# Performance work log

Hardware: AMD Instinct MI355X
Metric: run time of the kernel (lower is better)

## Reference

```python
import jax, jax.numpy as jnp
import numpy as np
from functools import partial

B, T, F = 4096, 256, 32
H1, H2, NT = 64, 32, 3


def _lstm_layer(x, W_ih, W_hh, b_ih, b_hh):
    """Torch-style LSTM (batch_first). x: [B,T,Fin], W_ih: [4H,Fin], W_hh: [4H,H].
    Gate order i, f, g, o. Returns all hidden states [B,T,H]."""
    Bsz = x.shape[0]
    H = W_hh.shape[1]
    # Precompute input contribution for all timesteps (one big GEMM)
    xg = jnp.einsum('btf,gf->btg', x, W_ih) + b_ih + b_hh  # [B,T,4H]

    def step(carry, xg_t):
        h, c = carry
        gates = xg_t + h @ W_hh.T  # [B,4H]
        i, f, g, o = jnp.split(gates, 4, axis=-1)
        i = jax.nn.sigmoid(i)
        f = jax.nn.sigmoid(f)
        g = jnp.tanh(g)
        o = jax.nn.sigmoid(o)
        c = f * c + i * g
        h = o * jnp.tanh(c)
        return (h, c), h

    init = (jnp.zeros((Bsz, H), x.dtype), jnp.zeros((Bsz, H), x.dtype))
    _, hs = jax.lax.scan(step, init, jnp.swapaxes(xg, 0, 1))  # hs: [T,B,H]
    return jnp.swapaxes(hs, 0, 1)


def setup_inputs() -> dict:
    key = jax.random.key(0)
    ks = jax.random.split(key, 12)
    s1 = 1.0 / np.sqrt(H1)
    s2 = 1.0 / np.sqrt(H2)
    u = lambda k, shape, s: jax.random.uniform(k, shape, jnp.float32, -s, s)
    return {
        'x': jax.random.normal(ks[0], (B, T, F), jnp.float32),
        'W_ih1': u(ks[1], (4 * H1, F), s1),
        'W_hh1': u(ks[2], (4 * H1, H1), s1),
        'b_ih1': u(ks[3], (4 * H1,), s1),
        'b_hh1': u(ks[4], (4 * H1,), s1),
        'W_ih2': u(ks[5], (4 * H2, H1), s2),
        'W_hh2': u(ks[6], (4 * H2, H2), s2),
        'b_ih2': u(ks[7], (4 * H2,), s2),
        'b_hh2': u(ks[8], (4 * H2,), s2),
        'W_head': u(ks[9], (NT, H2), s2),
        'b_head': u(ks[10], (NT,), s2),
    }


def reference(x, W_ih1, W_hh1, b_ih1, b_hh1, W_ih2, W_hh2, b_ih2, b_hh2, W_head, b_head):
    h1 = _lstm_layer(x, W_ih1, W_hh1, b_ih1, b_hh1)   # [B,T,64]; dropout is identity in eval
    h2 = _lstm_layer(h1, W_ih2, W_hh2, b_ih2, b_hh2)  # [B,T,32]
    last = h2[:, -1, :]                               # [B,32]
    return last @ W_head.T + b_head                   # [B,3]
```

## Files before the change

### kernel.cpp

```cpp
#include <hip/hip_runtime.h>

#define Bsz 4096
#define Tt  256
#define Ff  32
#define H1  64
#define H2  32
#define NTAPS 3
#define BT  16
#define NTHR 512
#define CH  16

typedef _Float16 half8  __attribute__((ext_vector_type(8)));
typedef __fp16   fp16x2 __attribute__((ext_vector_type(2)));
typedef float    f32x4  __attribute__((ext_vector_type(4)));

#define H1S 72
#define H2S 40
#define HDS 33

__device__ __forceinline__ float lstm_unit(float pi, float pf, float pg, float po,
                                           float& c) {
    const float K1 = 1.4426950408889634f;
    float ei = __builtin_amdgcn_exp2f(-K1 * pi);
    float ef = __builtin_amdgcn_exp2f(-K1 * pf);
    float eg = __builtin_amdgcn_exp2f(-2.0f * K1 * __builtin_fabsf(pg));
    float eo = __builtin_amdgcn_exp2f(-K1 * po);
    float p1 = (1.0f + ei) * (1.0f + eg);
    float pf1 = 1.0f + ef;
    float R  = __builtin_amdgcn_rcpf(p1 * pf1);
    float t1 = c * p1;
    float t2 = __builtin_copysignf(1.0f - eg, pg) * pf1;
    c = (t1 + t2) * R;
    float ec = __builtin_amdgcn_exp2f(-2.0f * K1 * __builtin_fabsf(c));
    float th = (1.0f - ec) * __builtin_amdgcn_rcpf((1.0f + eo) * (1.0f + ec));
    return __builtin_copysignf(th, c);
}

#define MFMA16(a, b, c) __builtin_amdgcn_mfma_f32_16x16x32_f16((a), (b), (c), 0, 0, 0)

__device__ __forceinline__ void dma16(const float* gp, const float* lp) {
    __builtin_amdgcn_global_load_lds(
        (const __attribute__((address_space(1))) void*)gp,
        (__attribute__((address_space(3))) void*)lp, 16, 0, 0);
}

__device__ __forceinline__ half8 cvt8(f32x4 lo, f32x4 hi) {
    union { half8 v; fp16x2 h[4]; } ax;
    ax.h[0] = __builtin_amdgcn_cvt_pkrtz(lo[0], lo[1]);
    ax.h[1] = __builtin_amdgcn_cvt_pkrtz(lo[2], lo[3]);
    ax.h[2] = __builtin_amdgcn_cvt_pkrtz(hi[0], hi[1]);
    ax.h[3] = __builtin_amdgcn_cvt_pkrtz(hi[2], hi[3]);
    return ax.v;
}

__global__ __launch_bounds__(NTHR, 2)
void lstm2_fused(const float* __restrict__ x,
                 const float* __restrict__ Wih1, const float* __restrict__ Whh1,
                 const float* __restrict__ bih1, const float* __restrict__ bhh1,
                 const float* __restrict__ Wih2, const float* __restrict__ Whh2,
                 const float* __restrict__ bih2, const float* __restrict__ bhh2,
                 const float* __restrict__ Whead, const float* __restrict__ bhead,
                 float* __restrict__ out)
{
    __shared__ __align__(16) _Float16 sH1[2][BT][H1S];
    __shared__ __align__(16) _Float16 sH2[2][BT][H2S];
    __shared__ __align__(16) float    sXC[2][CH][8][BT][4];
    __shared__ __align__(16) float    sXG[2][4][4][64][4];
    __shared__ __align__(16) float    sHead[BT][HDS];

    const int tid  = threadIdx.x;
    const int wid  = tid >> 6;
    const int lane = tid & 63;
    const int l15  = lane & 15;
    const int q    = lane >> 4;
    const int b0   = blockIdx.x * BT;
    const int u    = wid & 3;
    const bool isL1 = (wid < 4);

    const int hT = u & 1, rh = u >> 1;
    const int colL1 = u * 16 + l15;

    const int bL  = lane & 15;
    const int f4b = lane >> 4;
    const float* gbase = x + (size_t)(b0 + bL) * Tt * Ff;

    if (!isL1) {
        #pragma unroll
        for (int j = 0; j < 4; ++j) {
            int tl = u * 4 + j;
            #pragma unroll
            for (int h = 0; h < 2; ++h)
                dma16(gbase + (size_t)tl * Ff + (h * 4 + f4b) * 4,
                      &sXC[0][tl][h * 4][0][0]);
        }
    }

    half8 wA[4][3];
    half8 wX[4];
    float biasA[4], biasX[4];
    if (isL1) {
        #pragma unroll
        for (int G = 0; G < 4; ++G) {
            int gr = G * 64 + colL1;
            #pragma unroll
            for (int c = 0; c < 2; ++c) {
                half8 v;
                #pragma unroll
                for (int e = 0; e < 8; ++e)
                    v[e] = (_Float16)Whh1[gr * H1 + c * 32 + q * 8 + e];
                wA[G][c] = v;
            }
            wA[G][2] = wA[G][1];
            biasA[G] = 0.0f;
            biasX[G] = 0.0f;
        }
    } else {
        #pragma unroll
        for (int G = 0; G < 4; ++G) {
            int gr2 = G * 32 + hT * 16 + l15;
            half8 v0, v1, v2, vx;
            #pragma unroll
            for (int e = 0; e < 8; ++e) {
                int k = q * 8 + e;
                v0[e] = (_Float16)Whh2[gr2 * H2 + k];
                v1[e] = (_Float16)Wih2[gr2 * H1 + k];
                v2[e] = (_Float16)Wih2[gr2 * H1 + 32 + k];
            }
            wA[G][0] = v0; wA[G][1] = v1; wA[G][2] = v2;
            biasA[G] = bih2[gr2] + bhh2[gr2];

            int grx = G * 64 + u * 16 + l15;
            #pragma unroll
            for (int e = 0; e < 8; ++e)
                vx[e] = (_Float16)Wih1[grx * Ff + q * 8 + e];
            wX[G] = vx;
            biasX[G] = bih1[grx] + bhh1[grx];
        }
    }

    for (int idx = tid; idx < BT * H1S; idx += NTHR) ((_Float16*)sH1[1])[idx] = (_Float16)0.0f;
    for (int idx = tid; idx < BT * H2S; idx += NTHR) ((_Float16*)sH2[1])[idx] = (_Float16)0.0f;

    __syncthreads();

    if (!isL1) {
        f32x4 lo = *(const f32x4*)&sXC[0][0][2 * q][l15][0];
        f32x4 hi = *(const f32x4*)&sXC[0][0][2 * q + 1][l15][0];
        half8 ax = cvt8(lo, hi);
        #pragma unroll
        for (int G = 0; G < 4; ++G) {
            f32x4 a = {biasX[G], biasX[G], biasX[G], biasX[G]};
            a = MFMA16(ax, wX[G], a);
            *(f32x4*)&sXG[0][u][G][lane][0] = a;
        }
    }
    __syncthreads();

    float cs0 = 0.0f, cs1 = 0.0f, cs2 = 0.0f, cs3 = 0.0f;

    #pragma unroll 2
    for (int i = 0; i < Tt; ++i) {
        const int cur = i & 1, nxt = cur ^ 1;
        const int cbuf = (i >> 4) & 1;

        if (!isL1 && (i & (CH - 1)) == 0 && i + CH < Tt) {
            const float* gb = gbase + (size_t)(i + CH) * Ff;
            #pragma unroll
            for (int j = 0; j < 4; ++j) {
                int tl = u * 4 + j;
                #pragma unroll
                for (int h = 0; h < 2; ++h)
                    dma16(gb + (size_t)tl * Ff + (h * 4 + f4b) * 4,
                          &sXC[cbuf ^ 1][tl][h * 4][0][0]);
            }
        }

        half8 a0 = *(const half8*)&sH1[nxt][l15][q * 8];
        half8 a1 = *(const half8*)&sH1[nxt][l15][32 + q * 8];

        if (isL1) {
            f32x4 acc[4];
            #pragma unroll
            for (int G = 0; G < 4; ++G) {
                f32x4 a = *(const f32x4*)&sXG[cur][u][G][lane][0];
                a = MFMA16(a0, wA[G][0], a);
                a = MFMA16(a1, wA[G][1], a);
                acc[G] = a;
            }
            float h0 = lstm_unit(acc[0][0], acc[1][0], acc[2][0], acc[3][0], cs0);
            float h1v = lstm_unit(acc[0][1], acc[1][1], acc[2][1], acc[3][1], cs1);
            float h2v = lstm_unit(acc[0][2], acc[1][2], acc[2][2], acc[3][2], cs2);
            float h3v = lstm_unit(acc[0][3], acc[1][3], acc[2][3], acc[3][3], cs3);
            sH1[cur][q * 4 + 0][colL1] = (_Float16)h0;
            sH1[cur][q * 4 + 1][colL1] = (_Float16)h1v;
            sH1[cur][q * 4 + 2][colL1] = (_Float16)h2v;
            sH1[cur][q * 4 + 3][colL1] = (_Float16)h3v;
        } else {
            if (i >= 1) {
                half8 ah = *(const half8*)&sH2[cur][l15][q * 8];
                f32x4 acc[4];
                #pragma unroll
                for (int G = 0; G < 4; ++G) {
                    f32x4 a = {biasA[G], biasA[G], biasA[G], biasA[G]};
                    a = MFMA16(ah, wA[G][0], a);
                    a = MFMA16(a0, wA[G][1], a);
                    a = MFMA16(a1, wA[G][2], a);
                    acc[G] = a;
                }
                int r = rh * 2;
                float hA = lstm_unit(acc[0][r],     acc[1][r],     acc[2][r],     acc[3][r],     cs0);
                float hB = lstm_unit(acc[0][r + 1], acc[1][r + 1], acc[2][r + 1], acc[3][r + 1], cs1);
                sH2[nxt][q * 4 + r][hT * 16 + l15]     = (_Float16)hA;
                sH2[nxt][q * 4 + r + 1][hT * 16 + l15] = (_Float16)hB;
            }
            if (i + 1 < Tt) {
                const int t = i + 1, cb = (t >> 4) & 1, t16 = t & (CH - 1);
                f32x4 lo = *(const f32x4*)&sXC[cb][t16][2 * q][l15][0];
                f32x4 hi = *(const f32x4*)&sXC[cb][t16][2 * q + 1][l15][0];
                half8 ax = cvt8(lo, hi);
                #pragma unroll
                for (int G = 0; G < 4; ++G) {
                    f32x4 a = {biasX[G], biasX[G], biasX[G], biasX[G]};
                    a = MFMA16(ax, wX[G], a);
                    *(f32x4*)&sXG[nxt][u][G][lane][0] = a;
                }
            }
        }

        __syncthreads();
    }

    {
        const int cur = Tt & 1;
        const int nxt = cur ^ 1;
        if (!isL1) {
            half8 a0 = *(const half8*)&sH1[nxt][l15][q * 8];
            half8 a1 = *(const half8*)&sH1[nxt][l15][32 + q * 8];
            half8 ah = *(const half8*)&sH2[cur][l15][q * 8];
            f32x4 acc[4];
            #pragma unroll
            for (int G = 0; G < 4; ++G) {
                f32x4 a = {biasA[G], biasA[G], biasA[G], biasA[G]};
                a = MFMA16(ah, wA[G][0], a);
                a = MFMA16(a0, wA[G][1], a);
                a = MFMA16(a1, wA[G][2], a);
                acc[G] = a;
            }
            int r = rh * 2;
            float hA = lstm_unit(acc[0][r],     acc[1][r],     acc[2][r],     acc[3][r],     cs0);
            float hB = lstm_unit(acc[0][r + 1], acc[1][r + 1], acc[2][r + 1], acc[3][r + 1], cs1);
            sHead[q * 4 + r][hT * 16 + l15]     = hA;
            sHead[q * 4 + r + 1][hT * 16 + l15] = hB;
        }
        __syncthreads();
    }

    if (tid < BT * NTAPS) {
        int b = tid / NTAPS, n = tid - b * NTAPS;
        float s = bhead[n];
        #pragma unroll
        for (int k = 0; k < H2; ++k) s = fmaf(sHead[b][k], Whead[n * H2 + k], s);
        out[(size_t)(b0 + b) * NTAPS + n] = s;
    }
}

extern "C" void kernel_launch(void* const* d_in, const int* in_sizes, int n_in,
                              void* d_out, int out_size, void* d_ws, size_t ws_size,
                              hipStream_t stream) {
    const float* xp    = (const float*)d_in[0];
    const float* Wih1  = (const float*)d_in[1];
    const float* Whh1  = (const float*)d_in[2];
    const float* bih1  = (const float*)d_in[3];
    const float* bhh1  = (const float*)d_in[4];
    const float* Wih2  = (const float*)d_in[5];
    const float* Whh2  = (const float*)d_in[6];
    const float* bih2  = (const float*)d_in[7];
    const float* bhh2  = (const float*)d_in[8];
    const float* Whead = (const float*)d_in[9];
    const float* bhead = (const float*)d_in[10];
    float* outp = (float*)d_out;

    hipLaunchKernelGGL(lstm2_fused, dim3(Bsz / BT), dim3(NTHR), 0, stream,
                       xp, Wih1, Whh1, bih1, bhh1, Wih2, Whh2, bih2, bhh2,
                       Whead, bhead, outp);
}
```

Before: 392.3 us.

## Halve per-block batch tile to 8 rows and raise occupancy to four blocks

Cuts the batch rows per block from 16 to 8, which doubles the grid, and asks for four resident blocks per CU instead of two. The 16-row MFMA tiles now duplicate the 8 batch rows, so each lane evaluates fewer LSTM cell nonlinearities per step (layer 1 drops from four to two, layer 2 from two to one) and issues a single x DMA per timestep slot. The aim is to shorten the serial per-step critical path of the latency-bound recurrence and to hide the per-step barrier with more concurrent blocks. In exchange, half of every MFMA's work is redundant, so total matrix work per sample doubles, and the tighter launch bounds may force register spills.

```diff
diff --git a/kernel.cpp b/kernel.cpp
--- a/kernel.cpp
+++ b/kernel.cpp
@@ -6,7 +6,7 @@
 #define H1  64
 #define H2  32
 #define NTAPS 3
-#define BT  16
+#define BT  8
 #define NTHR 512
 #define CH  16
 
@@ -53,7 +53,7 @@
     return ax.v;
 }
 
-__global__ __launch_bounds__(NTHR, 2)
+__global__ __launch_bounds__(NTHR, 4)
 void lstm2_fused(const float* __restrict__ x,
                  const float* __restrict__ Wih1, const float* __restrict__ Whh1,
                  const float* __restrict__ bih1, const float* __restrict__ bhh1,
@@ -73,29 +73,31 @@
     const int lane = tid & 63;
     const int l15  = lane & 15;
     const int q    = lane >> 4;
+    const int row8 = l15 & 7;
     const int b0   = blockIdx.x * BT;
     const int u    = wid & 3;
     const bool isL1 = (wid < 4);
 
+    const int colL1 = u * 16 + l15;
+    const int r0  = (q >> 1) * 2, r1v = r0 + 1;
+    const int bLo = (q & 1) * 4 + (q >> 1) * 2;
     const int hT = u & 1, rh = u >> 1;
-    const int colL1 = u * 16 + l15;
-
-    const int bL  = lane & 15;
-    const int f4b = lane >> 4;
-    const float* gbase = x + (size_t)(b0 + bL) * Tt * Ff;
+    const int rL2 = (q >> 1) * 2 + rh;
+    const int bL2 = (q & 1) * 4 + (q >> 1) * 2 + rh;
+
+    const int bL  = lane & 7;
+    const int f4L = lane >> 3;
+    const float* gbase = x + (size_t)(b0 + bL) * Tt * Ff + f4L * 4;
 
     if (!isL1) {
         #pragma unroll
         for (int j = 0; j < 4; ++j) {
             int tl = u * 4 + j;
-            #pragma unroll
-            for (int h = 0; h < 2; ++h)
-                dma16(gbase + (size_t)tl * Ff + (h * 4 + f4b) * 4,
-                      &sXC[0][tl][h * 4][0][0]);
-        }
-    }
-
-    half8 wA[4][3];
+            dma16(gbase + (size_t)tl * Ff, &sXC[0][tl][0][0][0]);
+        }
+    }
+
+    half8 wL[4][3];
     half8 wX[4];
     float biasA[4], biasX[4];
     if (isL1) {
@@ -108,9 +110,9 @@
                 #pragma unroll
                 for (int e = 0; e < 8; ++e)
                     v[e] = (_Float16)Whh1[gr * H1 + c * 32 + q * 8 + e];
-                wA[G][c] = v;
-            }
-            wA[G][2] = wA[G][1];
+                wL[G][c] = v;
+            }
+            wL[G][2] = wL[G][1];
             biasA[G] = 0.0f;
             biasX[G] = 0.0f;
         }
@@ -126,7 +128,7 @@
                 v1[e] = (_Float16)Wih2[gr2 * H1 + k];
                 v2[e] = (_Float16)Wih2[gr2 * H1 + 32 + k];
             }
-            wA[G][0] = v0; wA[G][1] = v1; wA[G][2] = v2;
+            wL[G][0] = v0; wL[G][1] = v1; wL[G][2] = v2;
             biasA[G] = bih2[gr2] + bhh2[gr2];
 
             int grx = G * 64 + u * 16 + l15;
@@ -144,8 +146,8 @@
     __syncthreads();
 
     if (!isL1) {
-        f32x4 lo = *(const f32x4*)&sXC[0][0][2 * q][l15][0];
-        f32x4 hi = *(const f32x4*)&sXC[0][0][2 * q + 1][l15][0];
+        f32x4 lo = *(const f32x4*)&sXC[0][0][2 * q][row8][0];
+        f32x4 hi = *(const f32x4*)&sXC[0][0][2 * q + 1][row8][0];
         half8 ax = cvt8(lo, hi);
         #pragma unroll
         for (int G = 0; G < 4; ++G) {
@@ -156,7 +158,7 @@
     }
     __syncthreads();
 
-    float cs0 = 0.0f, cs1 = 0.0f, cs2 = 0.0f, cs3 = 0.0f;
+    float cs0 = 0.0f, cs1 = 0.0f;
 
     #pragma unroll 2
     for (int i = 0; i < Tt; ++i) {
@@ -168,55 +170,45 @@
             #pragma unroll
             for (int j = 0; j < 4; ++j) {
                 int tl = u * 4 + j;
-                #pragma unroll
-                for (int h = 0; h < 2; ++h)
-                    dma16(gb + (size_t)tl * Ff + (h * 4 + f4b) * 4,
-                          &sXC[cbuf ^ 1][tl][h * 4][0][0]);
-            }
-        }
-
-        half8 a0 = *(const half8*)&sH1[nxt][l15][q * 8];
-        half8 a1 = *(const half8*)&sH1[nxt][l15][32 + q * 8];
+                dma16(gb + (size_t)tl * Ff, &sXC[cbuf ^ 1][tl][0][0][0]);
+            }
+        }
+
+        half8 a0 = *(const half8*)&sH1[nxt][row8][q * 8];
+        half8 a1 = *(const half8*)&sH1[nxt][row8][32 + q * 8];
 
         if (isL1) {
             f32x4 acc[4];
             #pragma unroll
             for (int G = 0; G < 4; ++G) {
                 f32x4 a = *(const f32x4*)&sXG[cur][u][G][lane][0];
-                a = MFMA16(a0, wA[G][0], a);
-                a = MFMA16(a1, wA[G][1], a);
+                a = MFMA16(a0, wL[G][0], a);
+                a = MFMA16(a1, wL[G][1], a);
                 acc[G] = a;
             }
-            float h0 = lstm_unit(acc[0][0], acc[1][0], acc[2][0], acc[3][0], cs0);
-            float h1v = lstm_unit(acc[0][1], acc[1][1], acc[2][1], acc[3][1], cs1);
-            float h2v = lstm_unit(acc[0][2], acc[1][2], acc[2][2], acc[3][2], cs2);
-            float h3v = lstm_unit(acc[0][3], acc[1][3], acc[2][3], acc[3][3], cs3);
-            sH1[cur][q * 4 + 0][colL1] = (_Float16)h0;
-            sH1[cur][q * 4 + 1][colL1] = (_Float16)h1v;
-            sH1[cur][q * 4 + 2][colL1] = (_Float16)h2v;
-            sH1[cur][q * 4 + 3][colL1] = (_Float16)h3v;
+            float h0  = lstm_unit(acc[0][r0],  acc[1][r0],  acc[2][r0],  acc[3][r0],  cs0);
+            float h1v = lstm_unit(acc[0][r1v], acc[1][r1v], acc[2][r1v], acc[3][r1v], cs1);
+            sH1[cur][bLo][colL1]     = (_Float16)h0;
+            sH1[cur][bLo + 1][colL1] = (_Float16)h1v;
         } else {
             if (i >= 1) {
-                half8 ah = *(const half8*)&sH2[cur][l15][q * 8];
+                half8 ah = *(const half8*)&sH2[cur][row8][q * 8];
                 f32x4 acc[4];
                 #pragma unroll
                 for (int G = 0; G < 4; ++G) {
                     f32x4 a = {biasA[G], biasA[G], biasA[G], biasA[G]};
-                    a = MFMA16(ah, wA[G][0], a);
-                    a = MFMA16(a0, wA[G][1], a);
-                    a = MFMA16(a1, wA[G][2], a);
+                    a = MFMA16(ah, wL[G][0], a);
+                    a = MFMA16(a0, wL[G][1], a);
+                    a = MFMA16(a1, wL[G][2], a);
                     acc[G] = a;
                 }
-                int r = rh * 2;
-                float hA = lstm_unit(acc[0][r],     acc[1][r],     acc[2][r],     acc[3][r],     cs0);
-                float hB = lstm_unit(acc[0][r + 1], acc[1][r + 1], acc[2][r + 1], acc[3][r + 1], cs1);
-                sH2[nxt][q * 4 + r][hT * 16 + l15]     = (_Float16)hA;
-                sH2[nxt][q * 4 + r + 1][hT * 16 + l15] = (_Float16)hB;
+                float hA = lstm_unit(acc[0][rL2], acc[1][rL2], acc[2][rL2], acc[3][rL2], cs0);
+                sH2[nxt][bL2][hT * 16 + l15] = (_Float16)hA;
             }
             if (i + 1 < Tt) {
                 const int t = i + 1, cb = (t >> 4) & 1, t16 = t & (CH - 1);
-                f32x4 lo = *(const f32x4*)&sXC[cb][t16][2 * q][l15][0];
-                f32x4 hi = *(const f32x4*)&sXC[cb][t16][2 * q + 1][l15][0];
+                f32x4 lo = *(const f32x4*)&sXC[cb][t16][2 * q][row8][0];
+                f32x4 hi = *(const f32x4*)&sXC[cb][t16][2 * q + 1][row8][0];
                 half8 ax = cvt8(lo, hi);
                 #pragma unroll
                 for (int G = 0; G < 4; ++G) {
@@ -234,23 +226,20 @@
         const int cur = Tt & 1;
         const int nxt = cur ^ 1;
         if (!isL1) {
-            half8 a0 = *(const half8*)&sH1[nxt][l15][q * 8];
-            half8 a1 = *(const half8*)&sH1[nxt][l15][32 + q * 8];
-            half8 ah = *(const half8*)&sH2[cur][l15][q * 8];
+            half8 a0 = *(const half8*)&sH1[nxt][row8][q * 8];
+            half8 a1 = *(const half8*)&sH1[nxt][row8][32 + q * 8];
+            half8 ah = *(const half8*)&sH2[cur][row8][q * 8];
             f32x4 acc[4];
             #pragma unroll
             for (int G = 0; G < 4; ++G) {
                 f32x4 a = {biasA[G], biasA[G], biasA[G], biasA[G]};
-                a = MFMA16(ah, wA[G][0], a);
-                a = MFMA16(a0, wA[G][1], a);
-                a = MFMA16(a1, wA[G][2], a);
+                a = MFMA16(ah, wL[G][0], a);
+                a = MFMA16(a0, wL[G][1], a);
+                a = MFMA16(a1, wL[G][2], a);
                 acc[G] = a;
             }
-            int r = rh * 2;
-            float hA = lstm_unit(acc[0][r],     acc[1][r],     acc[2][r],     acc[3][r],     cs0);
-            float hB = lstm_unit(acc[0][r + 1], acc[1][r + 1], acc[2][r + 1], acc[3][r + 1], cs1);
-            sHead[q * 4 + r][hT * 16 + l15]     = hA;
-            sHead[q * 4 + r + 1][hT * 16 + l15] = hB;
+            float hA = lstm_unit(acc[0][rL2], acc[1][rL2], acc[2][rL2], acc[3][rL2], cs0);
+            sHead[bL2][hT * 16 + l15] = hA;
         }
         __syncthreads();
     }
```

Measured after the change: 471.6 us. 20.2% more time.
